# Kernel tuning notes

Hardware: AMD Instinct MI355X
Metric: run time of the kernel (lower is better)

## Reference

```python
import jax, jax.numpy as jnp
import numpy as np

EMB, HID, MEM, NQ = 768, 1024, 65536, 4096


def setup_inputs() -> dict:
    key = jax.random.key(0)
    ks = jax.random.split(key, 16)
    s = 0.02  # weight init scale to keep activations / softmax logits sane
    inp = {
        "query": jax.random.normal(ks[0], (NQ, EMB), jnp.float32),
        # input adapter: embedding_dim -> hidden_dim
        "W_in": jax.random.normal(ks[1], (EMB, HID), jnp.float32) * s,
        "b_in": jnp.zeros((HID,), jnp.float32),
        # encoder MLP: hidden -> 2*hidden -> hidden (GELU, dropout=eval noop)
        "W_e1": jax.random.normal(ks[2], (HID, 2 * HID), jnp.float32) * s,
        "b_e1": jnp.zeros((2 * HID,), jnp.float32),
        "W_e2": jax.random.normal(ks[3], (2 * HID, HID), jnp.float32) * s,
        "b_e2": jnp.zeros((HID,), jnp.float32),
        # memory_key projection
        "W_k": jax.random.normal(ks[4], (HID, HID), jnp.float32) * s,
        "b_k": jnp.zeros((HID,), jnp.float32),
        # learned memory bank (nn.Parameter ~ randn)
        "mem_keys": jax.random.normal(ks[5], (MEM, HID), jnp.float32),
        "mem_values": jax.random.normal(ks[6], (MEM, HID), jnp.float32),
        # retriever MLP: 2*hidden -> 2*hidden -> embedding_dim
        "W_r1": jax.random.normal(ks[7], (2 * HID, 2 * HID), jnp.float32) * s,
        "b_r1": jnp.zeros((2 * HID,), jnp.float32),
        "W_r2": jax.random.normal(ks[8], (2 * HID, EMB), jnp.float32) * s,
        "b_r2": jnp.zeros((EMB,), jnp.float32),
    }
    return inp


def reference(query, W_in, b_in, W_e1, b_e1, W_e2, b_e2, W_k, b_k,
              mem_keys, mem_values, W_r1, b_r1, W_r2, b_r2):
    # input adapter (embedding_dim -> hidden_dim)
    x = query @ W_in + b_in                                   # [NQ, HID]
    # encoder MLP (torch GELU default = exact erf)
    h = jax.nn.gelu(x @ W_e1 + b_e1, approximate=False)
    encoded = h @ W_e2 + b_e2                                  # [NQ, HID]
    # memory key projection
    key = encoded @ W_k + b_k                                  # [NQ, HID]
    # attention over the learned memory bank
    scale = 1.0 / jnp.sqrt(jnp.asarray(key.shape[-1], key.dtype))
    logits = (key @ mem_keys.T) * scale                        # [NQ, MEM]
    attn = jax.nn.softmax(logits, axis=-1)
    retrieved = attn @ mem_values                              # [NQ, HID]
    # concat + retriever MLP
    combined = jnp.concatenate([encoded, retrieved], axis=-1)  # [NQ, 2*HID]
    r = jax.nn.gelu(combined @ W_r1 + b_r1, approximate=False)
    result = r @ W_r2 + b_r2                                   # [NQ, EMB]
    return result
```

## Files before the change

kernel.cpp:

```cpp
#include <hip/hip_runtime.h>
#include <cstdint>
#include <cstddef>


#define EMB 768
#define HID 1024
#define MEMN 65536
#define NQ 4096
#define KSPLIT 8

typedef _Float16 half8 __attribute__((ext_vector_type(8)));
typedef _Float16 half4v __attribute__((ext_vector_type(4)));
typedef float float4v __attribute__((ext_vector_type(4)));


__global__ void cvt_f32_to_f16(const float* __restrict__ in,
                               _Float16* __restrict__ out, size_t n) {
  size_t i = ((size_t)blockIdx.x * blockDim.x + threadIdx.x) * 4;
  if (i >= n) return;
  float4 v = *(const float4*)(in + i);
  half4v h;
  h[0] = (_Float16)v.x; h[1] = (_Float16)v.y;
  h[2] = (_Float16)v.z; h[3] = (_Float16)v.w;
  *(half4v*)(out + i) = h;
}

__global__ void transpose_cvt(const float* __restrict__ in,
                              _Float16* __restrict__ out, int R, int C) {
  __shared__ float t[32][33];
  int tx = threadIdx.x, ty = threadIdx.y;
  int c0 = blockIdx.x * 32, r0 = blockIdx.y * 32;
#pragma unroll
  for (int k = 0; k < 4; ++k) {
    int r = r0 + ty + k * 8;
    t[ty + k * 8][tx] = in[(size_t)r * C + c0 + tx];
  }
  __syncthreads();
#pragma unroll
  for (int k = 0; k < 4; ++k) {
    int ro = c0 + ty + k * 8;
    out[(size_t)ro * R + r0 + tx] = (_Float16)t[tx][ty + k * 8];
  }
}

__global__ void transpose_cvt_f8(const float* __restrict__ in,
                                 uint8_t* __restrict__ out, int R, int C) {
  __shared__ float t[32][33];
  int tx = threadIdx.x, ty = threadIdx.y;
  int c0 = blockIdx.x * 32, r0 = blockIdx.y * 32;
#pragma unroll
  for (int k = 0; k < 4; ++k) {
    int r = r0 + ty + k * 8;
    t[ty + k * 8][tx] = in[(size_t)r * C + c0 + tx];
  }
  __syncthreads();
#pragma unroll
  for (int k = 0; k < 4; ++k) {
    int ro = c0 + ty + k * 8;
    float v = t[tx][ty + k * 8];
    int pk = __builtin_amdgcn_cvt_pk_fp8_f32(v, v, 0, false);
    out[(size_t)ro * R + r0 + tx] = (uint8_t)(pk & 0xff);
  }
}

__global__ void normalize_out(const float* __restrict__ O32,
                              const float* __restrict__ rs32,
                              _Float16* __restrict__ comb) {
  size_t i = ((size_t)blockIdx.x * blockDim.x + threadIdx.x) * 4;
  size_t row = i >> 10;
  size_t c = i & 1023;
  float4 v = *(const float4*)(O32 + i);
  float inv = 1.0f / rs32[row];
  half4v h;
  h[0] = (_Float16)(v.x * inv); h[1] = (_Float16)(v.y * inv);
  h[2] = (_Float16)(v.z * inv); h[3] = (_Float16)(v.w * inv);
  *(half4v*)(comb + row * 2048 + 1024 + c) = h;
}


enum { EPI_H16 = 0, EPI_GELU_H16 = 1, EPI_EXP_F8 = 2, EPI_F32 = 4 };

__device__ __forceinline__ void global_to_lds16(const void* g, void* l) {
  __builtin_amdgcn_global_load_lds(
      (const __attribute__((address_space(1))) void*)g,
      (__attribute__((address_space(3))) void*)l, 16, 0, 0);
}

__device__ __forceinline__ float gelu_erf(float x) {
  return 0.5f * x * (1.0f + erff(x * 0.7071067811865475f));
}

template <int EPI>
__global__ __launch_bounds__(256) void gemm_bt(
    const _Float16* __restrict__ A, int lda, const _Float16* __restrict__ BT,
    int ldb, const float* __restrict__ bias, void* __restrict__ Cout, int ldc,
    int K, float scale) {
  __shared__ __align__(16) _Float16 sA[128 * 64];
  __shared__ __align__(16) _Float16 sB[128 * 64];

  const int tid = threadIdx.x;
  const int lane = tid & 63;
  const int wave = tid >> 6;
  const int quad = lane >> 4;
  const int m16 = lane & 15;
  const int wm = (wave >> 1) * 64;
  const int wn = (wave & 1) * 64;

  const size_t rowBase = (size_t)blockIdx.y * 128;
  const size_t colBase = (size_t)blockIdx.x * 128;

  const int srow = lane >> 3;
  const int sg = (lane & 7) ^ srow;

  const _Float16* Abase[4];
  const _Float16* Bbase[4];
#pragma unroll
  for (int q = 0; q < 4; ++q) {
    int t = wave * 4 + q;
    Abase[q] = A + (rowBase + 8 * t + srow) * (size_t)lda + sg * 8;
    Bbase[q] = BT + (colBase + 8 * t + srow) * (size_t)ldb + sg * 8;
  }

  float4v acc[4][4] = {};

  for (int k0 = 0; k0 < K; k0 += 64) {
    __syncthreads();
#pragma unroll
    for (int q = 0; q < 4; ++q) {
      int t = wave * 4 + q;
      global_to_lds16(Abase[q] + k0, &sA[t * 512 + lane * 8]);
      global_to_lds16(Bbase[q] + k0, &sB[t * 512 + lane * 8]);
    }
    __syncthreads();

#pragma unroll
    for (int kk = 0; kk < 2; ++kk) {
      half8 af[4], bf[4];
      const int pg = kk * 4 + quad;
      const int ps = pg ^ (m16 & 7);
#pragma unroll
      for (int i = 0; i < 4; ++i)
        af[i] = *(const half8*)&sA[(wm + i * 16 + m16) * 64 + ps * 8];
#pragma unroll
      for (int j = 0; j < 4; ++j)
        bf[j] = *(const half8*)&sB[(wn + j * 16 + m16) * 64 + ps * 8];
#pragma unroll
      for (int i = 0; i < 4; ++i)
#pragma unroll
        for (int j = 0; j < 4; ++j)
          acc[i][j] =
              __builtin_amdgcn_mfma_f32_16x16x32_f16(af[i], bf[j], acc[i][j], 0, 0, 0);
    }
  }

#pragma unroll
  for (int i = 0; i < 4; ++i) {
#pragma unroll
    for (int j = 0; j < 4; ++j) {
      size_t c = colBase + wn + j * 16 + m16;
      float bv = (EPI == EPI_EXP_F8) ? 0.0f : bias[c];
#pragma unroll
      for (int rr = 0; rr < 4; ++rr) {
        size_t row = rowBase + wm + i * 16 + quad * 4 + rr;
        float x = acc[i][j][rr];
        if (EPI != EPI_EXP_F8) x += bv;
        if (EPI == EPI_GELU_H16) x = gelu_erf(x);
        if (EPI == EPI_EXP_F8) {
          x = expf(x * scale);
          int pk = __builtin_amdgcn_cvt_pk_fp8_f32(x, x, 0, false);
          ((uint8_t*)Cout)[row * (size_t)ldc + c] = (uint8_t)(pk & 0xff);
        } else if (EPI == EPI_F32) {
          ((float*)Cout)[row * (size_t)ldc + c] = x;
        } else {
          ((_Float16*)Cout)[row * (size_t)ldc + c] = (_Float16)x;
        }
      }
    }
  }
}

__global__ __launch_bounds__(256, 4) void gemm_pv_splitk_fp8(
    const uint8_t* __restrict__ P, const uint8_t* __restrict__ VT,
    float* __restrict__ O32, float* __restrict__ rs32, int Kslice,
    int mBlocks) {
  __shared__ __align__(16) uint8_t sA[2][128 * 64];
  __shared__ __align__(16) uint8_t sB[2][128 * 64];

  const int id = blockIdx.x;
  const int c8 = id & 7;
  const int nb = (id >> 3) & 7;
  const int g = (id >> 6) * 8 + c8;
  const int mb = g % mBlocks;
  const int ks = g / mBlocks;

  const int tid = threadIdx.x;
  const int lane = tid & 63;
  const int wave = tid >> 6;
  const int quad = lane >> 4;
  const int m16 = lane & 15;
  const int wm = (wave >> 1) * 64;
  const int wn = (wave & 1) * 64;

  const size_t rowBase = (size_t)mb * 128;
  const size_t colBase = (size_t)nb * 128;
  const int kBeg = ks * Kslice;

  const int srow = lane >> 2;
  const int g16 = lane & 3;
  const uint8_t* Asrc[2];
  const uint8_t* Bsrc[2];
  int dOff[2];
#pragma unroll
  for (int c = 0; c < 2; ++c) {
    int tr = wave * 32 + c * 16 + srow;
    int gs = g16 ^ ((tr >> 1) & 3);
    Asrc[c] = P + (rowBase + tr) * (size_t)MEMN + kBeg + gs * 16;
    Bsrc[c] = VT + (colBase + tr) * (size_t)MEMN + kBeg + gs * 16;
    dOff[c] = tr * 64 + g16 * 16;
  }

  auto stage = [&](int buf, int k0) {
#pragma unroll
    for (int c = 0; c < 2; ++c) {
      global_to_lds16(Asrc[c] + k0, &sA[buf][dOff[c]]);
      global_to_lds16(Bsrc[c] + k0, &sB[buf][dOff[c]]);
    }
  };

  float4v acc[4][4] = {};
  float4v accrs[4] = {};
  const bool doRS = (nb == 0) && ((wave & 1) == 0);
  const long vone = 0x3838383838383838L;

  const int nsteps = Kslice / 64;
  stage(0, 0);
  __syncthreads();

  int cur = 0;
  for (int step = 0; step < nsteps; ++step) {
    if (step + 1 < nsteps) stage(cur ^ 1, (step + 1) * 64);

#pragma unroll
    for (int kk = 0; kk < 2; ++kk) {
      const int g8 = (kk * 4 + quad) ^ (m16 & 6);
      long af[4], bf[4];
#pragma unroll
      for (int i = 0; i < 4; ++i)
        af[i] = *(const long*)&sA[cur][(wm + i * 16 + m16) * 64 + g8 * 8];
#pragma unroll
      for (int j = 0; j < 4; ++j)
        bf[j] = *(const long*)&sB[cur][(wn + j * 16 + m16) * 64 + g8 * 8];
#pragma unroll
      for (int i = 0; i < 4; ++i) {
#pragma unroll
        for (int j = 0; j < 4; ++j)
          acc[i][j] = __builtin_amdgcn_mfma_f32_16x16x32_fp8_fp8(
              af[i], bf[j], acc[i][j], 0, 0, 0);
        if (doRS)
          accrs[i] = __builtin_amdgcn_mfma_f32_16x16x32_fp8_fp8(
              af[i], vone, accrs[i], 0, 0, 0);
      }
    }

    __syncthreads();
    cur ^= 1;
  }

#pragma unroll
  for (int i = 0; i < 4; ++i) {
#pragma unroll
    for (int j = 0; j < 4; ++j) {
      size_t c = colBase + wn + j * 16 + m16;
#pragma unroll
      for (int rr = 0; rr < 4; ++rr) {
        size_t row = rowBase + wm + i * 16 + quad * 4 + rr;
        atomicAdd(&O32[row * 1024 + c], acc[i][j][rr]);
      }
    }
    if (doRS && m16 == 0) {
#pragma unroll
      for (int rr = 0; rr < 4; ++rr) {
        size_t row = rowBase + wm + i * 16 + quad * 4 + rr;
        atomicAdd(&rs32[row], accrs[i][rr]);
      }
    }
  }
}


static inline void* wsalloc(char*& p, size_t bytes) {
  void* r = (void*)p;
  p += (bytes + 255) & ~(size_t)255;
  return r;
}

extern "C" void kernel_launch(void* const* d_in, const int* in_sizes, int n_in,
                              void* d_out, int out_size, void* d_ws,
                              size_t ws_size, hipStream_t stream) {
  const float* query = (const float*)d_in[0];
  const float* W_in = (const float*)d_in[1];
  const float* b_in = (const float*)d_in[2];
  const float* W_e1 = (const float*)d_in[3];
  const float* b_e1 = (const float*)d_in[4];
  const float* W_e2 = (const float*)d_in[5];
  const float* b_e2 = (const float*)d_in[6];
  const float* W_k = (const float*)d_in[7];
  const float* b_k = (const float*)d_in[8];
  const float* memk = (const float*)d_in[9];
  const float* memv = (const float*)d_in[10];
  const float* W_r1 = (const float*)d_in[11];
  const float* b_r1 = (const float*)d_in[12];
  const float* W_r2 = (const float*)d_in[13];
  const float* b_r2 = (const float*)d_in[14];
  float* out = (float*)d_out;

  char* p = (char*)d_ws;
  _Float16* q16 = (_Float16*)wsalloc(p, (size_t)NQ * EMB * 2);
  _Float16* WinT = (_Float16*)wsalloc(p, (size_t)HID * EMB * 2);
  _Float16* We1T = (_Float16*)wsalloc(p, (size_t)2 * HID * HID * 2);
  _Float16* We2T = (_Float16*)wsalloc(p, (size_t)HID * 2 * HID * 2);
  _Float16* WkT = (_Float16*)wsalloc(p, (size_t)HID * HID * 2);
  _Float16* Wr1T = (_Float16*)wsalloc(p, (size_t)2 * HID * 2 * HID * 2);
  _Float16* Wr2T = (_Float16*)wsalloc(p, (size_t)EMB * 2 * HID * 2);
  _Float16* memk16 = (_Float16*)wsalloc(p, (size_t)MEMN * HID * 2);
  uint8_t* memvT8 = (uint8_t*)wsalloc(p, (size_t)HID * MEMN);
  _Float16* x16 = (_Float16*)wsalloc(p, (size_t)NQ * HID * 2);
  _Float16* h16 = (_Float16*)wsalloc(p, (size_t)NQ * 2 * HID * 2);
  _Float16* key16 = (_Float16*)wsalloc(p, (size_t)NQ * HID * 2);
  _Float16* comb16 = (_Float16*)wsalloc(p, (size_t)NQ * 2 * HID * 2);
  _Float16* r16 = (_Float16*)wsalloc(p, (size_t)NQ * 2 * HID * 2);
  float* O32 = (float*)wsalloc(p, (size_t)NQ * HID * 4);
  float* rs32 = (float*)wsalloc(p, (size_t)NQ * 4);

  size_t fixedBytes = (size_t)(p - (char*)d_ws);
  size_t Mc = NQ;
  while (Mc > 128 && fixedBytes + Mc * (size_t)MEMN > ws_size) Mc >>= 1;
  uint8_t* P8 = (uint8_t*)wsalloc(p, Mc * (size_t)MEMN);

  auto cvt = [&](const float* in, _Float16* o, size_t n) {
    cvt_f32_to_f16<<<dim3((unsigned)((n / 4 + 255) / 256)), 256, 0, stream>>>(in, o, n);
  };
  auto tr = [&](const float* in, _Float16* o, int R, int C) {
    transpose_cvt<<<dim3(C / 32, R / 32), dim3(32, 8), 0, stream>>>(in, o, R, C);
  };

  cvt(query, q16, (size_t)NQ * EMB);
  cvt(memk, memk16, (size_t)MEMN * HID);
  tr(W_in, WinT, EMB, HID);
  tr(W_e1, We1T, HID, 2 * HID);
  tr(W_e2, We2T, 2 * HID, HID);
  tr(W_k, WkT, HID, HID);
  tr(W_r1, Wr1T, 2 * HID, 2 * HID);
  tr(W_r2, Wr2T, 2 * HID, EMB);
  transpose_cvt_f8<<<dim3(HID / 32, MEMN / 32), dim3(32, 8), 0, stream>>>(
      memv, memvT8, MEMN, HID);

  gemm_bt<EPI_H16><<<dim3(HID / 128, NQ / 128), 256, 0, stream>>>(
      q16, EMB, WinT, EMB, b_in, x16, HID, EMB, 0.f);
  gemm_bt<EPI_GELU_H16><<<dim3(2 * HID / 128, NQ / 128), 256, 0, stream>>>(
      x16, HID, We1T, HID, b_e1, h16, 2 * HID, HID, 0.f);
  gemm_bt<EPI_H16><<<dim3(HID / 128, NQ / 128), 256, 0, stream>>>(
      h16, 2 * HID, We2T, 2 * HID, b_e2, comb16, 2 * HID, 2 * HID, 0.f);
  gemm_bt<EPI_H16><<<dim3(HID / 128, NQ / 128), 256, 0, stream>>>(
      comb16, 2 * HID, WkT, HID, b_k, key16, HID, HID, 0.f);

  hipMemsetAsync(O32, 0, (size_t)NQ * HID * 4, stream);
  hipMemsetAsync(rs32, 0, (size_t)NQ * 4, stream);

  const float scale = 0.03125f;
  const int Kslice = MEMN / KSPLIT;
  for (size_t m0 = 0; m0 < NQ; m0 += Mc) {
    gemm_bt<EPI_EXP_F8><<<dim3(MEMN / 128, (unsigned)(Mc / 128)), 256, 0, stream>>>(
        key16 + m0 * HID, HID, memk16, HID, nullptr, P8, MEMN, HID, scale);
    int mBlocks = (int)(Mc / 128);
    gemm_pv_splitk_fp8<<<dim3((unsigned)(mBlocks * KSPLIT * 8)), 256, 0, stream>>>(
        P8, memvT8, O32 + m0 * HID, rs32 + m0, Kslice, mBlocks);
  }

  normalize_out<<<dim3(NQ * HID / 4 / 256), 256, 0, stream>>>(O32, rs32, comb16);

  gemm_bt<EPI_GELU_H16><<<dim3(2 * HID / 128, NQ / 128), 256, 0, stream>>>(
      comb16, 2 * HID, Wr1T, 2 * HID, b_r1, r16, 2 * HID, 2 * HID, 0.f);
  gemm_bt<EPI_F32><<<dim3(EMB / 128, NQ / 128), 256, 0, stream>>>(
      r16, 2 * HID, Wr2T, 2 * HID, b_r2, out, EMB, 2 * HID, 0.f);

  (void)in_sizes; (void)n_in; (void)out_size;
}
```

Baseline: 2.071 ms.

## Run QK logits GEMM in FP8 with a dedicated double-buffered kernel

Converts memory keys and the projected query keys to FP8 and adds a dedicated FP8 MFMA kernel for the key-memory logits GEMM. It uses double-buffered LDS staging, XOR swizzling and grouped block ordering, with the exp and FP8 store fused into the epilogue. This halves the operand bytes and doubles MFMA throughput for the largest GEMM, and shrinks the memk conversion traffic. The cost is lower logit precision, since FP8 keys with randn memory keys could perturb the softmax accuracy.

```diff
diff --git a/kernel.cpp b/kernel.cpp
--- a/kernel.cpp
+++ b/kernel.cpp
@@ -23,6 +23,17 @@
   h[0] = (_Float16)v.x; h[1] = (_Float16)v.y;
   h[2] = (_Float16)v.z; h[3] = (_Float16)v.w;
   *(half4v*)(out + i) = h;
+}
+
+__global__ void cvt_f32_to_f8(const float* __restrict__ in,
+                              uint8_t* __restrict__ out, size_t n) {
+  size_t i = ((size_t)blockIdx.x * blockDim.x + threadIdx.x) * 4;
+  if (i >= n) return;
+  float4 v = *(const float4*)(in + i);
+  int lo = __builtin_amdgcn_cvt_pk_fp8_f32(v.x, v.y, 0, false);
+  int hi = __builtin_amdgcn_cvt_pk_fp8_f32(v.z, v.w, 0, false);
+  uint32_t w = (uint32_t)(lo & 0xffff) | ((uint32_t)hi << 16);
+  *(uint32_t*)(out + i) = w;
 }
 
 __global__ void transpose_cvt(const float* __restrict__ in,
@@ -78,7 +89,7 @@
 }
 
 
-enum { EPI_H16 = 0, EPI_GELU_H16 = 1, EPI_EXP_F8 = 2, EPI_F32 = 4 };
+enum { EPI_H16 = 0, EPI_GELU_H16 = 1, EPI_F32 = 4, EPI_H8 = 5 };
 
 __device__ __forceinline__ void global_to_lds16(const void* g, void* l) {
   __builtin_amdgcn_global_load_lds(
@@ -158,22 +169,114 @@
 #pragma unroll
     for (int j = 0; j < 4; ++j) {
       size_t c = colBase + wn + j * 16 + m16;
-      float bv = (EPI == EPI_EXP_F8) ? 0.0f : bias[c];
+      float bv = bias[c];
 #pragma unroll
       for (int rr = 0; rr < 4; ++rr) {
         size_t row = rowBase + wm + i * 16 + quad * 4 + rr;
-        float x = acc[i][j][rr];
-        if (EPI != EPI_EXP_F8) x += bv;
+        float x = acc[i][j][rr] + bv;
         if (EPI == EPI_GELU_H16) x = gelu_erf(x);
-        if (EPI == EPI_EXP_F8) {
-          x = expf(x * scale);
+        if (EPI == EPI_F32) {
+          ((float*)Cout)[row * (size_t)ldc + c] = x;
+        } else if (EPI == EPI_H8) {
           int pk = __builtin_amdgcn_cvt_pk_fp8_f32(x, x, 0, false);
           ((uint8_t*)Cout)[row * (size_t)ldc + c] = (uint8_t)(pk & 0xff);
-        } else if (EPI == EPI_F32) {
-          ((float*)Cout)[row * (size_t)ldc + c] = x;
         } else {
           ((_Float16*)Cout)[row * (size_t)ldc + c] = (_Float16)x;
         }
+      }
+    }
+  }
+  (void)scale;
+}
+
+__global__ __launch_bounds__(256, 4) void gemm_qk_fp8(
+    const uint8_t* __restrict__ A8, const uint8_t* __restrict__ BT8,
+    uint8_t* __restrict__ P8, int ny, float scale) {
+  __shared__ __align__(16) uint8_t sA[2][128 * 64];
+  __shared__ __align__(16) uint8_t sB[2][128 * 64];
+
+  const int id = blockIdx.x;
+  const int c8 = id & 7;
+  const int rest = id >> 3;
+  const int yb = rest % ny;
+  const int xb = (rest / ny) * 8 + c8;
+
+  const int tid = threadIdx.x;
+  const int lane = tid & 63;
+  const int wave = tid >> 6;
+  const int quad = lane >> 4;
+  const int m16 = lane & 15;
+  const int wm = (wave >> 1) * 64;
+  const int wn = (wave & 1) * 64;
+
+  const size_t rowBase = (size_t)yb * 128;
+  const size_t colBase = (size_t)xb * 128;
+
+  const int srow = lane >> 2;
+  const int g16 = lane & 3;
+  const uint8_t* Asrc[2];
+  const uint8_t* Bsrc[2];
+  int dOff[2];
+#pragma unroll
+  for (int c = 0; c < 2; ++c) {
+    int tr = wave * 32 + c * 16 + srow;
+    int gs = g16 ^ ((tr >> 1) & 3);
+    Asrc[c] = A8 + (rowBase + tr) * (size_t)HID + gs * 16;
+    Bsrc[c] = BT8 + (colBase + tr) * (size_t)HID + gs * 16;
+    dOff[c] = tr * 64 + g16 * 16;
+  }
+
+  auto stage = [&](int buf, int k0) {
+#pragma unroll
+    for (int c = 0; c < 2; ++c) {
+      global_to_lds16(Asrc[c] + k0, &sA[buf][dOff[c]]);
+      global_to_lds16(Bsrc[c] + k0, &sB[buf][dOff[c]]);
+    }
+  };
+
+  float4v acc[4][4] = {};
+
+  const int nsteps = HID / 64;
+  stage(0, 0);
+  __syncthreads();
+
+  int cur = 0;
+  for (int step = 0; step < nsteps; ++step) {
+    if (step + 1 < nsteps) stage(cur ^ 1, (step + 1) * 64);
+
+#pragma unroll
+    for (int kk = 0; kk < 2; ++kk) {
+      const int g8 = (kk * 4 + quad) ^ (m16 & 6);
+      long af[4], bf[4];
+#pragma unroll
+      for (int i = 0; i < 4; ++i)
+        af[i] = *(const long*)&sA[cur][(wm + i * 16 + m16) * 64 + g8 * 8];
+#pragma unroll
+      for (int j = 0; j < 4; ++j)
+        bf[j] = *(const long*)&sB[cur][(wn + j * 16 + m16) * 64 + g8 * 8];
+#pragma unroll
+      for (int i = 0; i < 4; ++i)
+#pragma unroll
+        for (int j = 0; j < 4; ++j)
+          acc[i][j] = __builtin_amdgcn_mfma_f32_16x16x32_fp8_fp8(
+              af[i], bf[j], acc[i][j], 0, 0, 0);
+    }
+
+    __syncthreads();
+    cur ^= 1;
+  }
+
+#pragma unroll
+  for (int i = 0; i < 4; ++i) {
+#pragma unroll
+    for (int j = 0; j < 4; ++j) {
+      size_t c = colBase + wn + j * 16 + m16;
+#pragma unroll
+      for (int rr = 0; rr < 4; ++rr) {
+        size_t row = rowBase + wm + i * 16 + quad * 4 + rr;
+        float x = expf(acc[i][j][rr] * scale);
+        int pk = __builtin_amdgcn_cvt_pk_fp8_f32(x, x, 0, false);
+        P8[row * (size_t)MEMN + c] = (uint8_t)(pk & 0xff);
       }
     }
   }
@@ -322,11 +425,11 @@
   _Float16* WkT = (_Float16*)wsalloc(p, (size_t)HID * HID * 2);
   _Float16* Wr1T = (_Float16*)wsalloc(p, (size_t)2 * HID * 2 * HID * 2);
   _Float16* Wr2T = (_Float16*)wsalloc(p, (size_t)EMB * 2 * HID * 2);
-  _Float16* memk16 = (_Float16*)wsalloc(p, (size_t)MEMN * HID * 2);
+  uint8_t* memk8 = (uint8_t*)wsalloc(p, (size_t)MEMN * HID);
   uint8_t* memvT8 = (uint8_t*)wsalloc(p, (size_t)HID * MEMN);
   _Float16* x16 = (_Float16*)wsalloc(p, (size_t)NQ * HID * 2);
   _Float16* h16 = (_Float16*)wsalloc(p, (size_t)NQ * 2 * HID * 2);
-  _Float16* key16 = (_Float16*)wsalloc(p, (size_t)NQ * HID * 2);
+  uint8_t* key8 = (uint8_t*)wsalloc(p, (size_t)NQ * HID);
   _Float16* comb16 = (_Float16*)wsalloc(p, (size_t)NQ * 2 * HID * 2);
   _Float16* r16 = (_Float16*)wsalloc(p, (size_t)NQ * 2 * HID * 2);
   float* O32 = (float*)wsalloc(p, (size_t)NQ * HID * 4);
@@ -345,7 +448,8 @@
   };
 
   cvt(query, q16, (size_t)NQ * EMB);
-  cvt(memk, memk16, (size_t)MEMN * HID);
+  cvt_f32_to_f8<<<dim3((unsigned)((size_t)MEMN * HID / 4 / 256)), 256, 0, stream>>>(
+      memk, memk8, (size_t)MEMN * HID);
   tr(W_in, WinT, EMB, HID);
   tr(W_e1, We1T, HID, 2 * HID);
   tr(W_e2, We2T, 2 * HID, HID);
@@ -361,8 +465,8 @@
       x16, HID, We1T, HID, b_e1, h16, 2 * HID, HID, 0.f);
   gemm_bt<EPI_H16><<<dim3(HID / 128, NQ / 128), 256, 0, stream>>>(
       h16, 2 * HID, We2T, 2 * HID, b_e2, comb16, 2 * HID, 2 * HID, 0.f);
-  gemm_bt<EPI_H16><<<dim3(HID / 128, NQ / 128), 256, 0, stream>>>(
-      comb16, 2 * HID, WkT, HID, b_k, key16, HID, HID, 0.f);
+  gemm_bt<EPI_H8><<<dim3(HID / 128, NQ / 128), 256, 0, stream>>>(
+      comb16, 2 * HID, WkT, HID, b_k, key8, HID, HID, 0.f);
 
   hipMemsetAsync(O32, 0, (size_t)NQ * HID * 4, stream);
   hipMemsetAsync(rs32, 0, (size_t)NQ * 4, stream);
@@ -370,11 +474,11 @@
   const float scale = 0.03125f;
   const int Kslice = MEMN / KSPLIT;
   for (size_t m0 = 0; m0 < NQ; m0 += Mc) {
-    gemm_bt<EPI_EXP_F8><<<dim3(MEMN / 128, (unsigned)(Mc / 128)), 256, 0, stream>>>(
-        key16 + m0 * HID, HID, memk16, HID, nullptr, P8, MEMN, HID, scale);
-    int mBlocks = (int)(Mc / 128);
-    gemm_pv_splitk_fp8<<<dim3((unsigned)(mBlocks * KSPLIT * 8)), 256, 0, stream>>>(
-        P8, memvT8, O32 + m0 * HID, rs32 + m0, Kslice, mBlocks);
+    int ny = (int)(Mc / 128);
+    gemm_qk_fp8<<<dim3((unsigned)(MEMN / 128 * ny)), 256, 0, stream>>>(
+        key8 + m0 * HID, memk8, P8, ny, scale);
+    gemm_pv_splitk_fp8<<<dim3((unsigned)(ny * KSPLIT * 8)), 256, 0, stream>>>(
+        P8, memvT8, O32 + m0 * HID, rs32 + m0, Kslice, ny);
   }
 
   normalize_out<<<dim3(NQ * HID / 4 / 256), 256, 0, stream>>>(O32, rs32, comb16);
```

New measurement: 1.845 ms. -10.9%, faster.
